# Performance work log

Measured on AMD Instinct MI355X. Metric: run time of the kernel, lower is better.

## Reference

```python
import jax, jax.numpy as jnp
import numpy as np

B, T = 1024, 128
LEN_VOCAB, IPD_VOCAB = 1500, 256
LEN_EB, IPD_EB = 64, 64
RNN_IN, HIDDEN, LABELS = 128, 512, 100


def setup_inputs() -> dict:
    key = jax.random.key(0)
    ks = jax.random.split(key, 11)
    std = 1.0 / np.sqrt(HIDDEN)

    def u(k, shape, s):
        return jax.random.uniform(k, shape, jnp.float32, -s, s)

    return {
        "x": jax.random.randint(ks[0], (B, T, 2), 0, 256, dtype=jnp.int64),
        "len_emb": jax.random.normal(ks[1], (LEN_VOCAB, LEN_EB), jnp.float32),
        "ipd_emb": jax.random.normal(ks[2], (IPD_VOCAB, IPD_EB), jnp.float32),
        "fc1_w": u(ks[3], (RNN_IN, LEN_EB + IPD_EB), 1.0 / np.sqrt(LEN_EB + IPD_EB)),
        "fc1_b": u(ks[4], (RNN_IN,), 1.0 / np.sqrt(LEN_EB + IPD_EB)),
        "x2h_w": u(ks[5], (HIDDEN, RNN_IN), std),
        "x2h_b": u(ks[6], (HIDDEN,), std),
        "h2h_w": u(ks[7], (HIDDEN, HIDDEN), std),
        "h2h_b": u(ks[8], (HIDDEN,), std),
        "fc2_w": u(ks[9], (LABELS, HIDDEN), 1.0 / np.sqrt(HIDDEN)),
        "fc2_b": u(ks[10], (LABELS,), 1.0 / np.sqrt(HIDDEN)),
    }


def reference(x, len_emb, ipd_emb, fc1_w, fc1_b, x2h_w, x2h_b, h2h_w, h2h_b, fc2_w, fc2_b):
    # Embedding lookups: [B, T, 64] each -> concat [B, T, 128]
    feats = jnp.concatenate([len_emb[x[:, :, 0]], ipd_emb[x[:, :, 1]]], axis=-1)
    # fc1 then precompute the x2h part of the recurrence for all timesteps
    r = feats @ fc1_w.T + fc1_b                       # [B, T, RNN_IN]
    xin = r @ x2h_w.T + x2h_b                         # [B, T, HIDDEN]
    xin_t = jnp.swapaxes(xin, 0, 1)                   # [T, B, HIDDEN]

    def step(h, xt):
        h = jnp.tanh(xt + h @ h2h_w.T + h2h_b)
        return h, None

    h0 = jnp.zeros((x.shape[0], h2h_w.shape[0]), dtype=xin.dtype)
    h_last, _ = jax.lax.scan(step, h0, xin_t)
    # eval mode: dropout is identity
    return h_last @ fc2_w.T + fc2_b                   # [B, LABELS]
```

## Files before the change

kernel.cpp:

```cpp
#include <hip/hip_runtime.h>

#define B_SZ 1024
#define T_SZ 128
#define HID 512
#define LAB 100

#define OFF_X     0u
#define OFF_WH    1048576u
#define OFF_LEN   1572864u
#define OFF_IPD   1764864u
#define OFF_FC2   1797632u
#define OFF_X2H   1900032u
#define OFF_FC2B  2031104u
#define OFF_XIN   2097152u
#define WS_NEED   136314880u

typedef __attribute__((ext_vector_type(8))) short short8;
typedef __attribute__((ext_vector_type(4))) float float4v;
typedef __attribute__((ext_vector_type(4))) unsigned short us4;
typedef __attribute__((ext_vector_type(8))) __bf16 bf8_t;
typedef unsigned long long ull;

__device__ __attribute__((aligned(16))) unsigned char g_blob[WS_NEED];

__device__ __forceinline__ float bf2f(unsigned short u) {
    union { unsigned int i; float f; } z; z.i = ((unsigned int)u) << 16; return z.f;
}
__device__ __forceinline__ unsigned short f2bf(float f) {
    union { float f; unsigned int i; } z; z.f = f;
    unsigned int r = z.i + 0x7FFFu + ((z.i >> 16) & 1u);
    return (unsigned short)(r >> 16);
}
__device__ __forceinline__ float4v mfma16(short8 a, short8 b, float4v c) {
    return __builtin_amdgcn_mfma_f32_16x16x32_bf16(
        __builtin_bit_cast(bf8_t, a), __builtin_bit_cast(bf8_t, b), c, 0, 0, 0);
}

__global__ void conv_x_kernel(const int* __restrict__ xi, int* __restrict__ xo) {
    __shared__ int is64;
    if (threadIdx.x == 0) {
        int nz = 0;
        for (int j = 1; j < 64; j += 2) nz |= xi[j];
        is64 = (nz == 0) ? 1 : 0;
    }
    __syncthreads();
    const int n = B_SZ * T_SZ * 2;
    const int i64 = is64;
    for (int i = blockIdx.x * blockDim.x + threadIdx.x; i < n; i += gridDim.x * blockDim.x) {
        int v = i64 ? xi[2 * i] : xi[i];
        v = v < 0 ? 0 : (v > 255 ? 255 : v);
        xo[i] = v;
    }
}

__global__ void conv_floats_kernel(const float* __restrict__ len_e, const float* __restrict__ ipd_e,
                                   const float* __restrict__ h2h, const float* __restrict__ fc2,
                                   const float* __restrict__ x2h, const float* __restrict__ fc2b,
                                   unsigned short* __restrict__ o_len, unsigned short* __restrict__ o_ipd,
                                   unsigned short* __restrict__ o_wh, unsigned short* __restrict__ o_fc2,
                                   unsigned short* __restrict__ o_x2h, float* __restrict__ o_fc2b) {
    const int N0 = 96000, N1 = 16384, N2 = 262144, N3 = 51200, N4 = 65536, N5 = 100;
    const int total = N0 + N1 + N2 + N3 + N4 + N5;
    for (int i = blockIdx.x * blockDim.x + threadIdx.x; i < total; i += gridDim.x * blockDim.x) {
        int j = i;
        if (j < N0) { o_len[j] = f2bf(len_e[j]); continue; }
        j -= N0;
        if (j < N1) { o_ipd[j] = f2bf(ipd_e[j]); continue; }
        j -= N1;
        if (j < N2) { o_wh[j] = f2bf(h2h[j]); continue; }
        j -= N2;
        if (j < N3) { o_fc2[j] = f2bf(fc2[j]); continue; }
        j -= N3;
        if (j < N4) { o_x2h[j] = f2bf(x2h[j]); continue; }
        j -= N4;
        o_fc2b[j] = fc2b[j];
    }
}

__launch_bounds__(256)
__global__ void xin_kernel(const int* __restrict__ w_x,
                           const unsigned short* __restrict__ w_len,
                           const unsigned short* __restrict__ w_ipd,
                           const float* __restrict__ fc1w, const float* __restrict__ fc1b,
                           const unsigned short* __restrict__ w_x2h,
                           const float* __restrict__ x2hb, const float* __restrict__ h2hb,
                           unsigned short* __restrict__ w_xin) {
    extern __shared__ unsigned short sm[];
    unsigned short* fT   = sm;
    unsigned short* fc1L = sm + 128 * 136;
    unsigned short* rT   = sm + 2 * 128 * 136;

    const int tid  = threadIdx.x;
    const int wv   = tid >> 6;
    const int ln   = tid & 63;
    const int mcol = ln & 15;
    const int q    = ln >> 4;
    const int t    = blockIdx.x >> 3;
    const int bg   = blockIdx.x & 7;

    {
        int row = tid >> 1, c = tid & 1;
        int idx = w_x[(bg * 128 + row) * 256 + t * 2 + c];
        const uint4* s4 = (const uint4*)((c ? w_ipd : w_len) + idx * 64);
        uint4* dst = (uint4*)&fT[row * 136 + c * 64];
#pragma unroll
        for (int i = 0; i < 8; i++) dst[i] = s4[i];
    }
#pragma unroll
    for (int it = 0; it < 8; it++) {
        int chunk = it * 256 + tid;
        int r = chunk >> 4, c8 = chunk & 15;
        const float* s = fc1w + r * 128 + c8 * 8;
        us4 a = { f2bf(s[0]), f2bf(s[1]), f2bf(s[2]), f2bf(s[3]) };
        us4 b = { f2bf(s[4]), f2bf(s[5]), f2bf(s[6]), f2bf(s[7]) };
        *(us4*)&fc1L[r * 136 + c8 * 8]     = a;
        *(us4*)&fc1L[r * 136 + c8 * 8 + 4] = b;
    }
    __syncthreads();

    for (int mt = 0; mt < 8; mt++) {
        float4v acc[2] = {{0.f,0.f,0.f,0.f},{0.f,0.f,0.f,0.f}};
#pragma unroll
        for (int kt = 0; kt < 4; kt++) {
            short8 bf = *(const short8*)&fT[(mt * 16 + mcol) * 136 + kt * 32 + q * 8];
#pragma unroll
            for (int u = 0; u < 2; u++) {
                int ntp = wv + u * 4;
                short8 fa = *(const short8*)&fc1L[(ntp * 16 + mcol) * 136 + kt * 32 + q * 8];
                acc[u] = mfma16(fa, bf, acc[u]);
            }
        }
#pragma unroll
        for (int u = 0; u < 2; u++) {
            int ntp = wv + u * 4;
            unsigned short o[4];
#pragma unroll
            for (int r = 0; r < 4; r++)
                o[r] = f2bf(acc[u][r] + fc1b[ntp * 16 + q * 4 + r]);
            us4 v = { o[0], o[1], o[2], o[3] };
            *(us4*)&rT[(mt * 16 + mcol) * 136 + ntp * 16 + q * 4] = v;
        }
    }
    __syncthreads();

    float bias[8][4];
#pragma unroll
    for (int i = 0; i < 8; i++)
#pragma unroll
        for (int r = 0; r < 4; r++) {
            int n = (wv * 8 + i) * 16 + q * 4 + r;
            bias[i][r] = x2hb[n] + h2hb[n];
        }
    for (int mt = 0; mt < 8; mt++) {
        float4v acc[8];
#pragma unroll
        for (int i = 0; i < 8; i++) acc[i] = (float4v){0.f,0.f,0.f,0.f};
#pragma unroll
        for (int kt = 0; kt < 4; kt++) {
            short8 bf = *(const short8*)&rT[(mt * 16 + mcol) * 136 + kt * 32 + q * 8];
#pragma unroll
            for (int i = 0; i < 8; i++) {
                int n16 = (wv * 8 + i) * 16;
                short8 fa = *(const short8*)(w_x2h + (n16 + mcol) * 128 + kt * 32 + q * 8);
                acc[i] = mfma16(fa, bf, acc[i]);
            }
        }
        int m = mt * 16 + mcol;
        int g = bg * 8 + (m >> 4), mm = m & 15;
#pragma unroll
        for (int i = 0; i < 8; i++) {
            int n0i = (wv * 8 + i) * 16 + q * 4;
            us4 v = { f2bf(acc[i][0] + bias[i][0]), f2bf(acc[i][1] + bias[i][1]),
                      f2bf(acc[i][2] + bias[i][2]), f2bf(acc[i][3] + bias[i][3]) };
            *(us4*)&w_xin[((t * 64 + g) * 16 + mm) * 512 + n0i] = v;
        }
    }
}

__launch_bounds__(512, 2)
__global__ void rnn_kernel(const unsigned short* __restrict__ w_wh,
                           const unsigned short* __restrict__ w_xin,
                           const unsigned short* __restrict__ w_fc2,
                           const float* __restrict__ w_fc2b,
                           float* __restrict__ out) {
    extern __shared__ unsigned short sm2[];
    unsigned short* sA = sm2;
    unsigned short* sH = sm2 + 65536;

    const int tid  = threadIdx.x;
    const int wv   = tid >> 6;
    const int ln   = tid & 63;
    const int mcol = ln & 15;
    const int q    = ln >> 4;
    const int g    = blockIdx.x;
    const int b0   = g * 16;
    const int n0   = wv * 64;

    for (int it = 0; it < 16; it++) {
        int chunk = it * 512 + tid;
        int r = chunk >> 4, c = chunk & 15;
        uint4 v = *(const uint4*)(w_wh + r * 512 + 384 + c * 8);
        *(uint4*)&sA[r * 128 + ((c ^ (r & 15)) & 15) * 8] = v;
    }
    {
        uint4 z = {0, 0, 0, 0};
        *(uint4*)&sH[tid * 8] = z;
        *(uint4*)&sH[(512 + tid) * 8] = z;
    }
    short8 whr[4][12];
#pragma unroll
    for (int nt = 0; nt < 4; nt++)
#pragma unroll
        for (int kt = 0; kt < 12; kt++)
            whr[nt][kt] = *(const short8*)(w_wh + (n0 + nt * 16 + mcol) * 512 + kt * 32 + q * 8);

    const int qlo = (q ^ (mcol & 3)) * 8;
    int ej[4];
#pragma unroll
    for (int j = 0; j < 4; j++)
        ej[j] = ((j * 4) ^ (mcol & 12)) * 8;
    const int base_b = mcol * 512 + qlo;
    const int fbase  = (n0 + mcol) * 128 + qlo;
    int hw_off[4];
#pragma unroll
    for (int nt = 0; nt < 4; nt++) {
        int n = n0 + nt * 16 + q * 4;
        hw_off[nt] = mcol * 512 + (((n >> 3) ^ mcol) & 63) * 8 + (n & 7);
    }

    const unsigned short* xin_p = w_xin + (g * 16 + mcol) * 512 + n0 + q * 4;
    us4 xq[4];
#pragma unroll
    for (int nt = 0; nt < 4; nt++)
        xq[nt] = *(const us4*)(xin_p + nt * 16);

    __syncthreads();

    for (int t = 0; t < T_SZ; t++) {
        const unsigned short* hRd = sH + ((t & 1) << 13);
        unsigned short* hWr = sH + (((t + 1) & 1) << 13);

        float4v acc[4];
#pragma unroll
        for (int nt = 0; nt < 4; nt++) {
            acc[nt][0] = bf2f(xq[nt][0]); acc[nt][1] = bf2f(xq[nt][1]);
            acc[nt][2] = bf2f(xq[nt][2]); acc[nt][3] = bf2f(xq[nt][3]);
        }
        xin_p += 64 * 16 * 512;
        if (t + 1 < T_SZ) {
#pragma unroll
            for (int nt = 0; nt < 4; nt++)
                xq[nt] = *(const us4*)(xin_p + nt * 16);
        }

#pragma unroll
        for (int kt = 0; kt < 12; kt++) {
            short8 bh = *(const short8*)&hRd[base_b + ej[kt & 3] + (kt >> 2) * 128];
#pragma unroll
            for (int nt = 0; nt < 4; nt++)
                acc[nt] = mfma16(whr[nt][kt], bh, acc[nt]);
        }
#pragma unroll
        for (int j = 0; j < 4; j++) {
            short8 bh = *(const short8*)&hRd[base_b + ej[j] + 384];
#pragma unroll
            for (int nt = 0; nt < 4; nt++) {
                short8 fa = *(const short8*)&sA[fbase + nt * 2048 + ej[j]];
                acc[nt] = mfma16(fa, bh, acc[nt]);
            }
        }

#pragma unroll
        for (int nt = 0; nt < 4; nt++) {
            unsigned short o[4];
#pragma unroll
            for (int r = 0; r < 4; r++) {
                float e  = __expf(2.0f * acc[nt][r]);
                float th = 1.0f - 2.0f * __builtin_amdgcn_rcpf(e + 1.0f);
                o[r] = f2bf(th);
            }
            us4 v4 = { o[0], o[1], o[2], o[3] };
            *(us4*)&hWr[hw_off[nt]] = v4;
        }
        __syncthreads();
    }

    unsigned short* hF = sH;

    if (wv < 7) {
        int lA = wv * 16 + mcol; if (lA > 99) lA = 99;
        float4v a2 = {0.f, 0.f, 0.f, 0.f};
#pragma unroll
        for (int kt = 0; kt < 16; kt++) {
            short8 fa = *(const short8*)(w_fc2 + lA * 512 + kt * 32 + q * 8);
            short8 bh = *(const short8*)&hF[base_b + ej[kt & 3] + (kt >> 2) * 128];
            a2 = mfma16(fa, bh, a2);
        }
#pragma unroll
        for (int r = 0; r < 4; r++) {
            int l = wv * 16 + q * 4 + r;
            if (l < 100) out[(b0 + mcol) * 100 + l] = a2[r] + w_fc2b[l];
        }
    }
}

extern "C" void kernel_launch(void* const* d_in, const int* in_sizes, int n_in,
                              void* d_out, int out_size, void* d_ws, size_t ws_size,
                              hipStream_t stream) {
    unsigned char* base = (unsigned char*)d_ws;
    if (ws_size < (size_t)WS_NEED) {
        void* p = nullptr;
        hipGetSymbolAddress(&p, HIP_SYMBOL(g_blob));
        base = (unsigned char*)p;
    }
    int*            w_x    = (int*)(base + OFF_X);
    unsigned short* w_wh   = (unsigned short*)(base + OFF_WH);
    unsigned short* w_len  = (unsigned short*)(base + OFF_LEN);
    unsigned short* w_ipd  = (unsigned short*)(base + OFF_IPD);
    unsigned short* w_fc2  = (unsigned short*)(base + OFF_FC2);
    unsigned short* w_x2h  = (unsigned short*)(base + OFF_X2H);
    float*          w_fc2b = (float*)(base + OFF_FC2B);
    unsigned short* w_xin  = (unsigned short*)(base + OFF_XIN);

    static bool attr_set = false;
    if (!attr_set) {
        hipFuncSetAttribute((const void*)xin_kernel,
                            hipFuncAttributeMaxDynamicSharedMemorySize, 3 * 128 * 136 * 2);
        hipFuncSetAttribute((const void*)rnn_kernel,
                            hipFuncAttributeMaxDynamicSharedMemorySize, 163840);
        attr_set = true;
    }

    conv_x_kernel<<<256, 256, 0, stream>>>((const int*)d_in[0], w_x);
    conv_floats_kernel<<<1024, 256, 0, stream>>>(
        (const float*)d_in[1], (const float*)d_in[2], (const float*)d_in[7],
        (const float*)d_in[9], (const float*)d_in[5], (const float*)d_in[10],
        w_len, w_ipd, w_wh, w_fc2, w_x2h, w_fc2b);
    xin_kernel<<<1024, 256, 3 * 128 * 136 * 2, stream>>>(
        w_x, w_len, w_ipd,
        (const float*)d_in[3], (const float*)d_in[4],
        w_x2h, (const float*)d_in[6], (const float*)d_in[8],
        w_xin);
    rnn_kernel<<<64, 512, 163840, stream>>>(
        w_wh, w_xin, w_fc2, w_fc2b, (float*)d_out);
}
```

Baseline: 401.2 us.

## Pre-convert fc1 weights once and shrink xin tiles to raise occupancy

fc1 weights are now converted to bf16 once in the conversion kernel and read straight from global memory, instead of every xin block converting them into shared memory. Each xin block now handles 64 batch rows instead of 128, so the grid doubles and shared memory per block drops from about 104KB to about 35KB, with launch bounds asking for 4 blocks per CU. The aim is higher occupancy and less redundant conversion work in the input-projection stage. The cost is more global reads of the fc1 and x2h weights, since each now-smaller block loads them separately.

```diff
diff --git a/kernel.cpp b/kernel.cpp
--- a/kernel.cpp
+++ b/kernel.cpp
@@ -12,6 +12,7 @@
 #define OFF_FC2   1797632u
 #define OFF_X2H   1900032u
 #define OFF_FC2B  2031104u
+#define OFF_FC1   2031616u
 #define OFF_XIN   2097152u
 #define WS_NEED   136314880u
 
@@ -56,11 +57,13 @@
 __global__ void conv_floats_kernel(const float* __restrict__ len_e, const float* __restrict__ ipd_e,
                                    const float* __restrict__ h2h, const float* __restrict__ fc2,
                                    const float* __restrict__ x2h, const float* __restrict__ fc2b,
+                                   const float* __restrict__ fc1,
                                    unsigned short* __restrict__ o_len, unsigned short* __restrict__ o_ipd,
                                    unsigned short* __restrict__ o_wh, unsigned short* __restrict__ o_fc2,
-                                   unsigned short* __restrict__ o_x2h, float* __restrict__ o_fc2b) {
-    const int N0 = 96000, N1 = 16384, N2 = 262144, N3 = 51200, N4 = 65536, N5 = 100;
-    const int total = N0 + N1 + N2 + N3 + N4 + N5;
+                                   unsigned short* __restrict__ o_x2h, float* __restrict__ o_fc2b,
+                                   unsigned short* __restrict__ o_fc1) {
+    const int N0 = 96000, N1 = 16384, N2 = 262144, N3 = 51200, N4 = 65536, N5 = 100, N6 = 16384;
+    const int total = N0 + N1 + N2 + N3 + N4 + N5 + N6;
     for (int i = blockIdx.x * blockDim.x + threadIdx.x; i < total; i += gridDim.x * blockDim.x) {
         int j = i;
         if (j < N0) { o_len[j] = f2bf(len_e[j]); continue; }
@@ -73,52 +76,44 @@
         j -= N3;
         if (j < N4) { o_x2h[j] = f2bf(x2h[j]); continue; }
         j -= N4;
-        o_fc2b[j] = fc2b[j];
-    }
-}
-
-__launch_bounds__(256)
+        if (j < N5) { o_fc2b[j] = fc2b[j]; continue; }
+        j -= N5;
+        o_fc1[j] = f2bf(fc1[j]);
+    }
+}
+
+__launch_bounds__(256, 4)
 __global__ void xin_kernel(const int* __restrict__ w_x,
                            const unsigned short* __restrict__ w_len,
                            const unsigned short* __restrict__ w_ipd,
-                           const float* __restrict__ fc1w, const float* __restrict__ fc1b,
+                           const unsigned short* __restrict__ w_fc1,
+                           const float* __restrict__ fc1b,
                            const unsigned short* __restrict__ w_x2h,
                            const float* __restrict__ x2hb, const float* __restrict__ h2hb,
                            unsigned short* __restrict__ w_xin) {
     extern __shared__ unsigned short sm[];
-    unsigned short* fT   = sm;
-    unsigned short* fc1L = sm + 128 * 136;
-    unsigned short* rT   = sm + 2 * 128 * 136;
+    unsigned short* fT = sm;
+    unsigned short* rT = sm + 64 * 136;
 
     const int tid  = threadIdx.x;
     const int wv   = tid >> 6;
     const int ln   = tid & 63;
     const int mcol = ln & 15;
     const int q    = ln >> 4;
-    const int t    = blockIdx.x >> 3;
-    const int bg   = blockIdx.x & 7;
-
-    {
+    const int t    = blockIdx.x >> 4;
+    const int bg   = blockIdx.x & 15;
+
+    if (tid < 128) {
         int row = tid >> 1, c = tid & 1;
-        int idx = w_x[(bg * 128 + row) * 256 + t * 2 + c];
+        int idx = w_x[(bg * 64 + row) * 256 + t * 2 + c];
         const uint4* s4 = (const uint4*)((c ? w_ipd : w_len) + idx * 64);
         uint4* dst = (uint4*)&fT[row * 136 + c * 64];
 #pragma unroll
         for (int i = 0; i < 8; i++) dst[i] = s4[i];
     }
-#pragma unroll
-    for (int it = 0; it < 8; it++) {
-        int chunk = it * 256 + tid;
-        int r = chunk >> 4, c8 = chunk & 15;
-        const float* s = fc1w + r * 128 + c8 * 8;
-        us4 a = { f2bf(s[0]), f2bf(s[1]), f2bf(s[2]), f2bf(s[3]) };
-        us4 b = { f2bf(s[4]), f2bf(s[5]), f2bf(s[6]), f2bf(s[7]) };
-        *(us4*)&fc1L[r * 136 + c8 * 8]     = a;
-        *(us4*)&fc1L[r * 136 + c8 * 8 + 4] = b;
-    }
     __syncthreads();
 
-    for (int mt = 0; mt < 8; mt++) {
+    for (int mt = 0; mt < 4; mt++) {
         float4v acc[2] = {{0.f,0.f,0.f,0.f},{0.f,0.f,0.f,0.f}};
 #pragma unroll
         for (int kt = 0; kt < 4; kt++) {
@@ -126,7 +121,7 @@
 #pragma unroll
             for (int u = 0; u < 2; u++) {
                 int ntp = wv + u * 4;
-                short8 fa = *(const short8*)&fc1L[(ntp * 16 + mcol) * 136 + kt * 32 + q * 8];
+                short8 fa = *(const short8*)(w_fc1 + (ntp * 16 + mcol) * 128 + kt * 32 + q * 8);
                 acc[u] = mfma16(fa, bf, acc[u]);
             }
         }
@@ -151,7 +146,7 @@
             int n = (wv * 8 + i) * 16 + q * 4 + r;
             bias[i][r] = x2hb[n] + h2hb[n];
         }
-    for (int mt = 0; mt < 8; mt++) {
+    for (int mt = 0; mt < 4; mt++) {
         float4v acc[8];
 #pragma unroll
         for (int i = 0; i < 8; i++) acc[i] = (float4v){0.f,0.f,0.f,0.f};
@@ -165,14 +160,13 @@
                 acc[i] = mfma16(fa, bf, acc[i]);
             }
         }
-        int m = mt * 16 + mcol;
-        int g = bg * 8 + (m >> 4), mm = m & 15;
+        int gidx = bg * 4 + mt;
 #pragma unroll
         for (int i = 0; i < 8; i++) {
             int n0i = (wv * 8 + i) * 16 + q * 4;
             us4 v = { f2bf(acc[i][0] + bias[i][0]), f2bf(acc[i][1] + bias[i][1]),
                       f2bf(acc[i][2] + bias[i][2]), f2bf(acc[i][3] + bias[i][3]) };
-            *(us4*)&w_xin[((t * 64 + g) * 16 + mm) * 512 + n0i] = v;
+            *(us4*)&w_xin[((t * 64 + gidx) * 16 + mcol) * 512 + n0i] = v;
         }
     }
 }
@@ -320,12 +314,13 @@
     unsigned short* w_fc2  = (unsigned short*)(base + OFF_FC2);
     unsigned short* w_x2h  = (unsigned short*)(base + OFF_X2H);
     float*          w_fc2b = (float*)(base + OFF_FC2B);
+    unsigned short* w_fc1  = (unsigned short*)(base + OFF_FC1);
     unsigned short* w_xin  = (unsigned short*)(base + OFF_XIN);
 
     static bool attr_set = false;
     if (!attr_set) {
         hipFuncSetAttribute((const void*)xin_kernel,
-                            hipFuncAttributeMaxDynamicSharedMemorySize, 3 * 128 * 136 * 2);
+                            hipFuncAttributeMaxDynamicSharedMemorySize, 2 * 64 * 136 * 2);
         hipFuncSetAttribute((const void*)rnn_kernel,
                             hipFuncAttributeMaxDynamicSharedMemorySize, 163840);
         attr_set = true;
@@ -335,10 +330,11 @@
     conv_floats_kernel<<<1024, 256, 0, stream>>>(
         (const float*)d_in[1], (const float*)d_in[2], (const float*)d_in[7],
         (const float*)d_in[9], (const float*)d_in[5], (const float*)d_in[10],
-        w_len, w_ipd, w_wh, w_fc2, w_x2h, w_fc2b);
-    xin_kernel<<<1024, 256, 3 * 128 * 136 * 2, stream>>>(
-        w_x, w_len, w_ipd,
-        (const float*)d_in[3], (const float*)d_in[4],
+        (const float*)d_in[3],
+        w_len, w_ipd, w_wh, w_fc2, w_x2h, w_fc2b, w_fc1);
+    xin_kernel<<<2048, 256, 2 * 64 * 136 * 2, stream>>>(
+        w_x, w_len, w_ipd, w_fc1,
+        (const float*)d_in[4],
         w_x2h, (const float*)d_in[6], (const float*)d_in[8],
         w_xin);
     rnn_kernel<<<64, 512, 163840, stream>>>(
```

New measurement: 504.0 us. 25.6% more time.

## Fuse xin precompute and RNN into one kernel with counter-based streaming

Applied to the files above, without the earlier changes.

Merges the xin projection kernel and the recurrent kernel into a single launch. The first 64 blocks run the RNN and the remaining 1024 blocks compute xin per timestep, signalling completion through per-group atomic counters. The RNN blocks spin-wait on these counters every 8 timesteps, so the recurrence can start before all of xin is written. This removes a kernel boundary and overlaps the projection with the serial recurrence. In exchange, the xin blocks now launch with 512 threads and 160KB of shared memory while using only half the threads, which lowers their occupancy. Forward progress also depends on the 64 RNN blocks not starving the producer blocks of CU slots.

```diff
diff --git a/kernel.cpp b/kernel.cpp
--- a/kernel.cpp
+++ b/kernel.cpp
@@ -12,6 +12,7 @@
 #define OFF_FC2   1797632u
 #define OFF_X2H   1900032u
 #define OFF_FC2B  2031104u
+#define OFF_CNT   2031616u
 #define OFF_XIN   2097152u
 #define WS_NEED   136314880u
 
@@ -36,7 +37,9 @@
         __builtin_bit_cast(bf8_t, a), __builtin_bit_cast(bf8_t, b), c, 0, 0, 0);
 }
 
-__global__ void conv_x_kernel(const int* __restrict__ xi, int* __restrict__ xo) {
+__global__ void conv_x_kernel(const int* __restrict__ xi, int* __restrict__ xo,
+                              unsigned int* __restrict__ cnt) {
+    if (blockIdx.x == 0 && threadIdx.x < 16) cnt[threadIdx.x] = 0u;
     __shared__ int is64;
     if (threadIdx.x == 0) {
         int nz = 0;
@@ -77,121 +80,129 @@
     }
 }
 
-__launch_bounds__(256)
-__global__ void xin_kernel(const int* __restrict__ w_x,
-                           const unsigned short* __restrict__ w_len,
-                           const unsigned short* __restrict__ w_ipd,
-                           const float* __restrict__ fc1w, const float* __restrict__ fc1b,
-                           const unsigned short* __restrict__ w_x2h,
-                           const float* __restrict__ x2hb, const float* __restrict__ h2hb,
-                           unsigned short* __restrict__ w_xin) {
+__launch_bounds__(512, 2)
+__global__ void fused_kernel(const int* __restrict__ w_x,
+                             const unsigned short* __restrict__ w_len,
+                             const unsigned short* __restrict__ w_ipd,
+                             const float* __restrict__ fc1w, const float* __restrict__ fc1b,
+                             const unsigned short* __restrict__ w_x2h,
+                             const float* __restrict__ x2hb, const float* __restrict__ h2hb,
+                             unsigned short* __restrict__ w_xin,
+                             const unsigned short* __restrict__ w_wh,
+                             const unsigned short* __restrict__ w_fc2,
+                             const float* __restrict__ w_fc2b,
+                             float* __restrict__ out,
+                             unsigned int* __restrict__ cnt) {
     extern __shared__ unsigned short sm[];
-    unsigned short* fT   = sm;
-    unsigned short* fc1L = sm + 128 * 136;
-    unsigned short* rT   = sm + 2 * 128 * 136;
-
     const int tid  = threadIdx.x;
     const int wv   = tid >> 6;
     const int ln   = tid & 63;
     const int mcol = ln & 15;
     const int q    = ln >> 4;
-    const int t    = blockIdx.x >> 3;
-    const int bg   = blockIdx.x & 7;
-
-    {
-        int row = tid >> 1, c = tid & 1;
-        int idx = w_x[(bg * 128 + row) * 256 + t * 2 + c];
-        const uint4* s4 = (const uint4*)((c ? w_ipd : w_len) + idx * 64);
-        uint4* dst = (uint4*)&fT[row * 136 + c * 64];
-#pragma unroll
-        for (int i = 0; i < 8; i++) dst[i] = s4[i];
-    }
-#pragma unroll
-    for (int it = 0; it < 8; it++) {
-        int chunk = it * 256 + tid;
-        int r = chunk >> 4, c8 = chunk & 15;
-        const float* s = fc1w + r * 128 + c8 * 8;
-        us4 a = { f2bf(s[0]), f2bf(s[1]), f2bf(s[2]), f2bf(s[3]) };
-        us4 b = { f2bf(s[4]), f2bf(s[5]), f2bf(s[6]), f2bf(s[7]) };
-        *(us4*)&fc1L[r * 136 + c8 * 8]     = a;
-        *(us4*)&fc1L[r * 136 + c8 * 8 + 4] = b;
-    }
-    __syncthreads();
-
-    for (int mt = 0; mt < 8; mt++) {
-        float4v acc[2] = {{0.f,0.f,0.f,0.f},{0.f,0.f,0.f,0.f}};
-#pragma unroll
-        for (int kt = 0; kt < 4; kt++) {
-            short8 bf = *(const short8*)&fT[(mt * 16 + mcol) * 136 + kt * 32 + q * 8];
-#pragma unroll
-            for (int u = 0; u < 2; u++) {
-                int ntp = wv + u * 4;
-                short8 fa = *(const short8*)&fc1L[(ntp * 16 + mcol) * 136 + kt * 32 + q * 8];
-                acc[u] = mfma16(fa, bf, acc[u]);
-            }
-        }
-#pragma unroll
-        for (int u = 0; u < 2; u++) {
-            int ntp = wv + u * 4;
-            unsigned short o[4];
-#pragma unroll
-            for (int r = 0; r < 4; r++)
-                o[r] = f2bf(acc[u][r] + fc1b[ntp * 16 + q * 4 + r]);
-            us4 v = { o[0], o[1], o[2], o[3] };
-            *(us4*)&rT[(mt * 16 + mcol) * 136 + ntp * 16 + q * 4] = v;
-        }
-    }
-    __syncthreads();
-
-    float bias[8][4];
-#pragma unroll
-    for (int i = 0; i < 8; i++)
-#pragma unroll
-        for (int r = 0; r < 4; r++) {
-            int n = (wv * 8 + i) * 16 + q * 4 + r;
-            bias[i][r] = x2hb[n] + h2hb[n];
-        }
-    for (int mt = 0; mt < 8; mt++) {
-        float4v acc[8];
-#pragma unroll
-        for (int i = 0; i < 8; i++) acc[i] = (float4v){0.f,0.f,0.f,0.f};
-#pragma unroll
-        for (int kt = 0; kt < 4; kt++) {
-            short8 bf = *(const short8*)&rT[(mt * 16 + mcol) * 136 + kt * 32 + q * 8];
-#pragma unroll
-            for (int i = 0; i < 8; i++) {
-                int n16 = (wv * 8 + i) * 16;
-                short8 fa = *(const short8*)(w_x2h + (n16 + mcol) * 128 + kt * 32 + q * 8);
-                acc[i] = mfma16(fa, bf, acc[i]);
-            }
-        }
-        int m = mt * 16 + mcol;
-        int g = bg * 8 + (m >> 4), mm = m & 15;
-#pragma unroll
-        for (int i = 0; i < 8; i++) {
-            int n0i = (wv * 8 + i) * 16 + q * 4;
-            us4 v = { f2bf(acc[i][0] + bias[i][0]), f2bf(acc[i][1] + bias[i][1]),
-                      f2bf(acc[i][2] + bias[i][2]), f2bf(acc[i][3] + bias[i][3]) };
-            *(us4*)&w_xin[((t * 64 + g) * 16 + mm) * 512 + n0i] = v;
-        }
-    }
-}
-
-__launch_bounds__(512, 2)
-__global__ void rnn_kernel(const unsigned short* __restrict__ w_wh,
-                           const unsigned short* __restrict__ w_xin,
-                           const unsigned short* __restrict__ w_fc2,
-                           const float* __restrict__ w_fc2b,
-                           float* __restrict__ out) {
-    extern __shared__ unsigned short sm2[];
-    unsigned short* sA = sm2;
-    unsigned short* sH = sm2 + 65536;
-
-    const int tid  = threadIdx.x;
-    const int wv   = tid >> 6;
-    const int ln   = tid & 63;
-    const int mcol = ln & 15;
-    const int q    = ln >> 4;
+
+    if (blockIdx.x >= 64) {
+        const int xbid = blockIdx.x - 64;
+        const int t  = xbid >> 3;
+        const int bg = xbid & 7;
+        unsigned short* fT   = sm;
+        unsigned short* fc1L = sm + 128 * 136;
+        unsigned short* rT   = sm + 2 * 128 * 136;
+
+        if (tid < 256) {
+            {
+                int row = tid >> 1, c = tid & 1;
+                int idx = w_x[(bg * 128 + row) * 256 + t * 2 + c];
+                const uint4* s4 = (const uint4*)((c ? w_ipd : w_len) + idx * 64);
+                uint4* dst = (uint4*)&fT[row * 136 + c * 64];
+#pragma unroll
+                for (int i = 0; i < 8; i++) dst[i] = s4[i];
+            }
+#pragma unroll
+            for (int it = 0; it < 8; it++) {
+                int chunk = it * 256 + tid;
+                int r = chunk >> 4, c8 = chunk & 15;
+                const float* s = fc1w + r * 128 + c8 * 8;
+                us4 a = { f2bf(s[0]), f2bf(s[1]), f2bf(s[2]), f2bf(s[3]) };
+                us4 b = { f2bf(s[4]), f2bf(s[5]), f2bf(s[6]), f2bf(s[7]) };
+                *(us4*)&fc1L[r * 136 + c8 * 8]     = a;
+                *(us4*)&fc1L[r * 136 + c8 * 8 + 4] = b;
+            }
+        }
+        __syncthreads();
+
+        if (tid < 256) {
+            for (int mt = 0; mt < 8; mt++) {
+                float4v acc[2] = {{0.f,0.f,0.f,0.f},{0.f,0.f,0.f,0.f}};
+#pragma unroll
+                for (int kt = 0; kt < 4; kt++) {
+                    short8 bf = *(const short8*)&fT[(mt * 16 + mcol) * 136 + kt * 32 + q * 8];
+#pragma unroll
+                    for (int u = 0; u < 2; u++) {
+                        int ntp = wv + u * 4;
+                        short8 fa = *(const short8*)&fc1L[(ntp * 16 + mcol) * 136 + kt * 32 + q * 8];
+                        acc[u] = mfma16(fa, bf, acc[u]);
+                    }
+                }
+#pragma unroll
+                for (int u = 0; u < 2; u++) {
+                    int ntp = wv + u * 4;
+                    unsigned short o[4];
+#pragma unroll
+                    for (int r = 0; r < 4; r++)
+                        o[r] = f2bf(acc[u][r] + fc1b[ntp * 16 + q * 4 + r]);
+                    us4 v = { o[0], o[1], o[2], o[3] };
+                    *(us4*)&rT[(mt * 16 + mcol) * 136 + ntp * 16 + q * 4] = v;
+                }
+            }
+        }
+        __syncthreads();
+
+        if (tid < 256) {
+            float bias[8][4];
+#pragma unroll
+            for (int i = 0; i < 8; i++)
+#pragma unroll
+                for (int r = 0; r < 4; r++) {
+                    int n = (wv * 8 + i) * 16 + q * 4 + r;
+                    bias[i][r] = x2hb[n] + h2hb[n];
+                }
+            for (int mt = 0; mt < 8; mt++) {
+                float4v acc[8];
+#pragma unroll
+                for (int i = 0; i < 8; i++) acc[i] = (float4v){0.f,0.f,0.f,0.f};
+#pragma unroll
+                for (int kt = 0; kt < 4; kt++) {
+                    short8 bf = *(const short8*)&rT[(mt * 16 + mcol) * 136 + kt * 32 + q * 8];
+#pragma unroll
+                    for (int i = 0; i < 8; i++) {
+                        int n16 = (wv * 8 + i) * 16;
+                        short8 fa = *(const short8*)(w_x2h + (n16 + mcol) * 128 + kt * 32 + q * 8);
+                        acc[i] = mfma16(fa, bf, acc[i]);
+                    }
+                }
+                int m = mt * 16 + mcol;
+                int g = bg * 8 + (m >> 4), mm = m & 15;
+#pragma unroll
+                for (int i = 0; i < 8; i++) {
+                    int n0i = (wv * 8 + i) * 16 + q * 4;
+                    us4 v = { f2bf(acc[i][0] + bias[i][0]), f2bf(acc[i][1] + bias[i][1]),
+                              f2bf(acc[i][2] + bias[i][2]), f2bf(acc[i][3] + bias[i][3]) };
+                    *(us4*)&w_xin[((t * 64 + g) * 16 + mm) * 512 + n0i] = v;
+                }
+            }
+        }
+        __syncthreads();
+        if (tid == 0) {
+            __threadfence();
+            __hip_atomic_fetch_add(&cnt[t >> 3], 1u,
+                                   __ATOMIC_RELEASE, __HIP_MEMORY_SCOPE_SYSTEM);
+        }
+        return;
+    }
+
+    unsigned short* sA = sm;
+    unsigned short* sH = sm + 65536;
+
     const int g    = blockIdx.x;
     const int b0   = g * 16;
     const int n0   = wv * 64;
@@ -228,15 +239,30 @@
         hw_off[nt] = mcol * 512 + (((n >> 3) ^ mcol) & 63) * 8 + (n & 7);
     }
 
+    if (tid == 0) {
+        while (__hip_atomic_load(&cnt[0], __ATOMIC_RELAXED, __HIP_MEMORY_SCOPE_SYSTEM) < 64u)
+            __builtin_amdgcn_s_sleep(16);
+        __threadfence();
+    }
+    __syncthreads();
+
     const unsigned short* xin_p = w_xin + (g * 16 + mcol) * 512 + n0 + q * 4;
     us4 xq[4];
 #pragma unroll
     for (int nt = 0; nt < 4; nt++)
         xq[nt] = *(const us4*)(xin_p + nt * 16);
 
-    __syncthreads();
-
     for (int t = 0; t < T_SZ; t++) {
+        if ((((t + 1) & 7) == 0) && (t + 1) < T_SZ) {
+            if (tid == 0) {
+                const int gp = (t + 1) >> 3;
+                while (__hip_atomic_load(&cnt[gp], __ATOMIC_RELAXED, __HIP_MEMORY_SCOPE_SYSTEM) < 64u)
+                    __builtin_amdgcn_s_sleep(16);
+                __threadfence();
+            }
+            __syncthreads();
+        }
+
         const unsigned short* hRd = sH + ((t & 1) << 13);
         unsigned short* hWr = sH + (((t + 1) & 1) << 13);
 
@@ -320,27 +346,25 @@
     unsigned short* w_fc2  = (unsigned short*)(base + OFF_FC2);
     unsigned short* w_x2h  = (unsigned short*)(base + OFF_X2H);
     float*          w_fc2b = (float*)(base + OFF_FC2B);
+    unsigned int*   w_cnt  = (unsigned int*)(base + OFF_CNT);
     unsigned short* w_xin  = (unsigned short*)(base + OFF_XIN);
 
     static bool attr_set = false;
     if (!attr_set) {
-        hipFuncSetAttribute((const void*)xin_kernel,
-                            hipFuncAttributeMaxDynamicSharedMemorySize, 3 * 128 * 136 * 2);
-        hipFuncSetAttribute((const void*)rnn_kernel,
+        hipFuncSetAttribute((const void*)fused_kernel,
                             hipFuncAttributeMaxDynamicSharedMemorySize, 163840);
         attr_set = true;
     }
 
-    conv_x_kernel<<<256, 256, 0, stream>>>((const int*)d_in[0], w_x);
+    conv_x_kernel<<<256, 256, 0, stream>>>((const int*)d_in[0], w_x, w_cnt);
     conv_floats_kernel<<<1024, 256, 0, stream>>>(
         (const float*)d_in[1], (const float*)d_in[2], (const float*)d_in[7],
         (const float*)d_in[9], (const float*)d_in[5], (const float*)d_in[10],
         w_len, w_ipd, w_wh, w_fc2, w_x2h, w_fc2b);
-    xin_kernel<<<1024, 256, 3 * 128 * 136 * 2, stream>>>(
+    fused_kernel<<<1088, 512, 163840, stream>>>(
         w_x, w_len, w_ipd,
         (const float*)d_in[3], (const float*)d_in[4],
         w_x2h, (const float*)d_in[6], (const float*)d_in[8],
-        w_xin);
-    rnn_kernel<<<64, 512, 163840, stream>>>(
-        w_wh, w_xin, w_fc2, w_fc2b, (float*)d_out);
-}
+        w_xin,
+        w_wh, w_fc2, w_fc2b, (float*)d_out, w_cnt);
+}
```

Result: no change. 405.3 us (+1.0%).
